# Performance work log

Hardware: AMD Instinct MI355X
Metric: run time of the kernel (lower is better)

The kernel has to match this reference:

```python
import jax, jax.numpy as jnp
import numpy as np

H = 16  # num_heads


def rope_cos_sin(S, d):
    # interleaved RoPE tables: cos = [cos0,cos0,cos1,cos1,...], sin likewise
    pos = jnp.arange(S, dtype=jnp.float32)[:, None]            # [S,1]
    ids = jnp.arange(d // 2, dtype=jnp.float32)
    theta = jnp.power(10000.0, -2.0 * ids / d)                  # [d/2]
    ang = pos * theta                                           # [S,d/2]
    cos = jnp.repeat(jnp.cos(ang), 2, axis=-1)                  # [S,d]
    sin = jnp.repeat(jnp.sin(ang), 2, axis=-1)                  # [S,d]
    return cos, sin


def apply_rope(x, cos, sin):
    # x: [B,H,S,d]; x2 = [-x1, x0, -x3, x2, ...]
    x2 = jnp.stack([-x[..., 1::2], x[..., ::2]], axis=-1).reshape(x.shape)
    return x * cos + x2 * sin


def setup_inputs() -> dict:
    key = jax.random.key(0)
    ks = jax.random.split(key, 9)
    B, S, D = 2, 2048, 1024
    sc = 1.0 / np.sqrt(D)
    return {
        "x": jax.random.normal(ks[0], (B, S, D), dtype=jnp.float32),
        "Wq": jax.random.normal(ks[1], (D, D), dtype=jnp.float32) * sc,
        "bq": jnp.zeros((D,), dtype=jnp.float32),
        "Wk": jax.random.normal(ks[2], (D, D), dtype=jnp.float32) * sc,
        "bk": jnp.zeros((D,), dtype=jnp.float32),
        "Wv": jax.random.normal(ks[3], (D, D), dtype=jnp.float32) * sc,
        "bv": jnp.zeros((D,), dtype=jnp.float32),
        "Wo": jax.random.normal(ks[4], (D, D), dtype=jnp.float32) * sc,
        "bo": jnp.zeros((D,), dtype=jnp.float32),
    }


def reference(x, Wq, bq, Wk, bk, Wv, bv, Wo, bo):
    B, S, D = x.shape
    dk = D // H
    scale = dk ** -0.5  # lsa=False -> fixed scale
    # QKV projections -> [B,H,S,dk]
    q = (x @ Wq + bq).reshape(B, S, H, dk).transpose(0, 2, 1, 3)
    k = (x @ Wk + bk).reshape(B, S, H, dk).transpose(0, 2, 1, 3)
    v = (x @ Wv + bv).reshape(B, S, H, dk).transpose(0, 2, 1, 3)
    cos, sin = rope_cos_sin(S, dk)
    q = apply_rope(q, cos, sin)
    k = apply_rope(k, cos, sin)
    attn_scores = jnp.einsum('bhqd,bhkd->bhqk', q, k) * scale
    attn_weights = jax.nn.softmax(attn_scores, axis=-1)  # dropout p=0
    out = jnp.einsum('bhqk,bhkd->bhqd', attn_weights, v)
    out = out.transpose(0, 2, 1, 3).reshape(B, S, D)
    out = out @ Wo + bo
    return out, attn_weights
```

## Files before the change

### kernel.cpp

```cpp
#include <hip/hip_runtime.h>

typedef __attribute__((ext_vector_type(4))) float f32x4;
typedef __attribute__((ext_vector_type(4))) int   i32x4;
typedef __attribute__((ext_vector_type(8))) short bf16x8;
typedef __attribute__((ext_vector_type(4))) short s16x4;

#define HD 16
#define SQ 2048
#define DM 1024
#define DK 64
#define QSCALE 0.18033688011112042f

__device__ __forceinline__ short f2bf(float f){
  union { float f; unsigned u; } c; c.f = f;
  unsigned r = (c.u + 0x7FFFu + ((c.u >> 16) & 1u)) >> 16;
  return (short)r;
}
__device__ __forceinline__ f32x4 mfma16(bf16x8 a, bf16x8 b, f32x4 c){
  return __builtin_amdgcn_mfma_f32_16x16x32_bf16(a, b, c, 0, 0, 0);
}
__device__ __forceinline__ void gload16(const void* g, void* l){
  __builtin_amdgcn_global_load_lds(
      (const __attribute__((address_space(1))) unsigned*)g,
      (__attribute__((address_space(3))) unsigned*)l, 16, 0, 0);
}


__global__ void k_rope_tab(float2* __restrict__ tab){
  int i = blockIdx.x * 256 + threadIdx.x;
  int s = i >> 5, d2 = i & 31;
  float theta = powf(10000.0f, -(float)d2 / 32.0f);
  float ang = (float)s * theta;
  tab[i] = make_float2(cosf(ang), sinf(ang));
}

__global__ void k_cast(const float* __restrict__ x, short* __restrict__ xb){
  int i = (blockIdx.x * 256 + threadIdx.x) * 4;
  f32x4 v = *(const f32x4*)(x + i);
  s16x4 o;
  o[0] = f2bf(v[0]); o[1] = f2bf(v[1]); o[2] = f2bf(v[2]); o[3] = f2bf(v[3]);
  *(s16x4*)(xb + i) = o;
}

__global__ void k_wt4(const float* __restrict__ W0, const float* __restrict__ W1,
                      const float* __restrict__ W2, const float* __restrict__ W3,
                      short* __restrict__ T0, short* __restrict__ T1,
                      short* __restrict__ T2, short* __restrict__ T3){
  __shared__ float t[32][33];
  const float* W; short* Wt;
  if (blockIdx.z == 0)      { W = W0; Wt = T0; }
  else if (blockIdx.z == 1) { W = W1; Wt = T1; }
  else if (blockIdx.z == 2) { W = W2; Wt = T2; }
  else                      { W = W3; Wt = T3; }
  int kx = blockIdx.x * 32, nx = blockIdx.y * 32;
  int lx = threadIdx.x & 31, ly = threadIdx.x >> 5;
#pragma unroll
  for (int i = 0; i < 32; i += 8)
    t[ly + i][lx] = W[(size_t)(kx + ly + i) * DM + nx + lx];
  __syncthreads();
#pragma unroll
  for (int i = 0; i < 32; i += 8)
    Wt[(size_t)(nx + ly + i) * DM + kx + lx] = f2bf(t[lx][ly + i]);
}

__global__ __launch_bounds__(256) void k_projqkv(const short* __restrict__ A,
    const short* __restrict__ Wqt, const short* __restrict__ Wkt, const short* __restrict__ Wvt,
    const float* __restrict__ bq, const float* __restrict__ bk, const float* __restrict__ bv,
    const float2* __restrict__ rope,
    short* __restrict__ Qo, short* __restrict__ Ko, short* __restrict__ Vo)
{
  __shared__ short As[128 * 64];
  __shared__ short Bs[128 * 64];
  const int mat = blockIdx.y >> 3;
  const int n0 = (blockIdx.y & 7) * 128;
  const short* Bt  = (mat == 0) ? Wqt : (mat == 1) ? Wkt : Wvt;
  const float* bias = (mat == 0) ? bq : (mat == 1) ? bk : bv;
  const int tid = threadIdx.x;
  const int lane = tid & 63, w = tid >> 6;
  const int wr = w >> 1, wc = w & 1;
  const int l15 = lane & 15, l4 = lane >> 4;
  const int m0 = blockIdx.x * 128;
  f32x4 acc[4][4] = {};

  for (int k0 = 0; k0 < DM; k0 += 64) {
#pragma unroll
    for (int i = 0; i < 4; ++i) {
      int c = w * 4 + i;
      int row = c * 8 + (lane >> 3);
      int so = (((lane & 7) * 16) ^ ((row & 7) << 4)) >> 1;
      gload16(A  + (size_t)(m0 + row) * DM + k0 + so, (char*)As + c * 1024);
      gload16(Bt + (size_t)(n0 + row) * DM + k0 + so, (char*)Bs + c * 1024);
    }
    __syncthreads();
#pragma unroll
    for (int kk = 0; kk < 64; kk += 32) {
      bf16x8 af[4], bfr[4];
#pragma unroll
      for (int mi = 0; mi < 4; ++mi) {
        int r = wr * 64 + mi * 16 + l15;
        af[mi] = *(const bf16x8*)((char*)As + ((r * 128 + kk * 2 + l4 * 16) ^ ((r & 7) << 4)));
      }
#pragma unroll
      for (int ni = 0; ni < 4; ++ni) {
        int r = wc * 64 + ni * 16 + l15;
        bfr[ni] = *(const bf16x8*)((char*)Bs + ((r * 128 + kk * 2 + l4 * 16) ^ ((r & 7) << 4)));
      }
#pragma unroll
      for (int mi = 0; mi < 4; ++mi)
#pragma unroll
        for (int ni = 0; ni < 4; ++ni)
          acc[mi][ni] = mfma16(af[mi], bfr[ni], acc[mi][ni]);
    }
    __syncthreads();
  }

#pragma unroll
  for (int mi = 0; mi < 4; ++mi) {
#pragma unroll
    for (int ni = 0; ni < 4; ++ni) {
      int n = n0 + wc * 64 + ni * 16 + l15;
      float bv2 = bias[n];
      if (mat == 2) {
        s16x4 pk;
        int mb = m0 + wr * 64 + mi * 16 + l4 * 4;
#pragma unroll
        for (int r2 = 0; r2 < 4; ++r2) pk[r2] = f2bf(acc[mi][ni][r2] + bv2);
        int b = mb >> 11, s = mb & 2047, h = n >> 6, d = n & 63;
        *(s16x4*)(Vo + ((size_t)((b * HD + h) * DK + d)) * SQ + s) = pk;
      } else {
        short* outp = (mat == 0) ? Qo : Ko;
        float sc = (mat == 0) ? QSCALE : 1.0f;
#pragma unroll
        for (int r2 = 0; r2 < 4; ++r2) {
          int m = m0 + wr * 64 + mi * 16 + l4 * 4 + r2;
          float v = acc[mi][ni][r2] + bv2;
          float pr = __shfl_xor(v, 1);
          int s = m & 2047, d = n & 63;
          float2 cs = rope[(s << 5) + (d >> 1)];
          v = (d & 1) ? (v * cs.x + pr * cs.y) : (v * cs.x - pr * cs.y);
          v *= sc;
          int b = m >> 11, h = n >> 6;
          outp[((size_t)((b * HD + h) * SQ + s)) * DK + d] = f2bf(v);
        }
      }
    }
  }
}

__global__ __launch_bounds__(256) void k_projO(const short* __restrict__ A, const short* __restrict__ Bt,
                                               const float* __restrict__ bias, float* __restrict__ out)
{
  __shared__ short As[64 * 64];
  __shared__ short Bs[128 * 64];
  const int tid = threadIdx.x;
  const int lane = tid & 63, w = tid >> 6;
  const int wr = w >> 1, wc = w & 1;
  const int l15 = lane & 15, l4 = lane >> 4;
  const int m0 = blockIdx.x * 64, n0 = blockIdx.y * 128;
  f32x4 acc[2][4] = {};

  for (int k0 = 0; k0 < DM; k0 += 64) {
#pragma unroll
    for (int i = 0; i < 2; ++i) {
      int c = w * 2 + i;
      int row = c * 8 + (lane >> 3);
      int so = (((lane & 7) * 16) ^ ((row & 7) << 4)) >> 1;
      gload16(A + (size_t)(m0 + row) * DM + k0 + so, (char*)As + c * 1024);
    }
#pragma unroll
    for (int i = 0; i < 4; ++i) {
      int c = w * 4 + i;
      int row = c * 8 + (lane >> 3);
      int so = (((lane & 7) * 16) ^ ((row & 7) << 4)) >> 1;
      gload16(Bt + (size_t)(n0 + row) * DM + k0 + so, (char*)Bs + c * 1024);
    }
    __syncthreads();
#pragma unroll
    for (int kk = 0; kk < 64; kk += 32) {
      bf16x8 af[2], bfr[4];
#pragma unroll
      for (int mi = 0; mi < 2; ++mi) {
        int r = wr * 32 + mi * 16 + l15;
        af[mi] = *(const bf16x8*)((char*)As + ((r * 128 + kk * 2 + l4 * 16) ^ ((r & 7) << 4)));
      }
#pragma unroll
      for (int ni = 0; ni < 4; ++ni) {
        int r = wc * 64 + ni * 16 + l15;
        bfr[ni] = *(const bf16x8*)((char*)Bs + ((r * 128 + kk * 2 + l4 * 16) ^ ((r & 7) << 4)));
      }
#pragma unroll
      for (int mi = 0; mi < 2; ++mi)
#pragma unroll
        for (int ni = 0; ni < 4; ++ni)
          acc[mi][ni] = mfma16(af[mi], bfr[ni], acc[mi][ni]);
    }
    __syncthreads();
  }

#pragma unroll
  for (int mi = 0; mi < 2; ++mi)
#pragma unroll
    for (int ni = 0; ni < 4; ++ni) {
      int n = n0 + wc * 64 + ni * 16 + l15;
      float bv2 = bias[n];
#pragma unroll
      for (int r2 = 0; r2 < 4; ++r2) {
        int m = m0 + wr * 32 + mi * 16 + l4 * 4 + r2;
        out[(size_t)m * DM + n] = acc[mi][ni][r2] + bv2;
      }
    }
}

__global__ __launch_bounds__(256) void k_attn2(const short* __restrict__ Q, const short* __restrict__ K,
    const short* __restrict__ Vt, float* __restrict__ attn_out, short* __restrict__ ctx)
{
  __shared__ short Qs[128 * 64];
  __shared__ short Ks[128 * 64];
  __shared__ short Vs[64 * 128];
  __shared__ short Ps[128 * 128];
  const int bh = blockIdx.y, qt = blockIdx.x;
  const int tid = threadIdx.x, lane = tid & 63, w = tid >> 6;
  const int l15 = lane & 15, l4 = lane >> 4;
  const short* Qg = Q + (size_t)(bh * SQ + qt * 128) * DK;
  const short* Kg = K + (size_t)bh * SQ * DK;
  const short* Vg = Vt + (size_t)bh * DK * SQ;

#pragma unroll
  for (int i = 0; i < 4; ++i) {
    int c = w * 4 + i;
    int row = c * 8 + (lane >> 3);
    int so = (((lane & 7) * 16) ^ ((row & 7) << 4)) >> 1;
    gload16(Qg + row * 64 + so, (char*)Qs + c * 1024);
  }

  float rs[2][4] = {};
  for (int kt = 0; kt < 16; ++kt) {
#pragma unroll
    for (int i = 0; i < 4; ++i) {
      int c = w * 4 + i;
      int row = c * 8 + (lane >> 3);
      int so = (((lane & 7) * 16) ^ ((row & 7) << 4)) >> 1;
      gload16(Kg + (size_t)(kt * 128 + row) * 64 + so, (char*)Ks + c * 1024);
    }
    __syncthreads();
    f32x4 p[2][8] = {};
#pragma unroll
    for (int kk = 0; kk < 64; kk += 32) {
      bf16x8 aq[2];
#pragma unroll
      for (int mi = 0; mi < 2; ++mi) {
        int r = w * 32 + mi * 16 + l15;
        aq[mi] = *(const bf16x8*)((char*)Qs + ((r * 128 + kk * 2 + l4 * 16) ^ ((r & 7) << 4)));
      }
#pragma unroll
      for (int ni = 0; ni < 8; ++ni) {
        int r = ni * 16 + l15;
        bf16x8 bk = *(const bf16x8*)((char*)Ks + ((r * 128 + kk * 2 + l4 * 16) ^ ((r & 7) << 4)));
        p[0][ni] = mfma16(aq[0], bk, p[0][ni]);
        p[1][ni] = mfma16(aq[1], bk, p[1][ni]);
      }
    }
#pragma unroll
    for (int mi = 0; mi < 2; ++mi)
#pragma unroll
      for (int ni = 0; ni < 8; ++ni)
#pragma unroll
        for (int r2 = 0; r2 < 4; ++r2)
          rs[mi][r2] += exp2f(p[mi][ni][r2]);
    __syncthreads();
  }
  float rinv_r[2][4];
#pragma unroll
  for (int mi = 0; mi < 2; ++mi)
#pragma unroll
    for (int r2 = 0; r2 < 4; ++r2) {
      float v = rs[mi][r2];
      v += __shfl_xor(v, 1); v += __shfl_xor(v, 2);
      v += __shfl_xor(v, 4); v += __shfl_xor(v, 8);
      rinv_r[mi][r2] = 1.0f / v;
    }

  f32x4 c[2][4] = {};
  float* attn_base = attn_out + ((size_t)(bh * SQ + qt * 128)) * SQ;

  for (int kt = 0; kt < 16; ++kt) {
#pragma unroll
    for (int i = 0; i < 4; ++i) {
      int c2 = w * 4 + i;
      int row = c2 * 8 + (lane >> 3);
      int so = (((lane & 7) * 16) ^ ((row & 7) << 4)) >> 1;
      gload16(Kg + (size_t)(kt * 128 + row) * 64 + so, (char*)Ks + c2 * 1024);
    }
#pragma unroll
    for (int i = 0; i < 4; ++i) {
      int c2 = w * 4 + i;
      int row = c2 * 4 + (lane >> 4);
      int so = (((lane & 15) * 16) ^ ((row & 15) << 4)) >> 1;
      gload16(Vg + (size_t)row * SQ + kt * 128 + so, (char*)Vs + c2 * 1024);
    }
    __syncthreads();
    f32x4 p[2][8] = {};
#pragma unroll
    for (int kk = 0; kk < 64; kk += 32) {
      bf16x8 aq[2];
#pragma unroll
      for (int mi = 0; mi < 2; ++mi) {
        int r = w * 32 + mi * 16 + l15;
        aq[mi] = *(const bf16x8*)((char*)Qs + ((r * 128 + kk * 2 + l4 * 16) ^ ((r & 7) << 4)));
      }
#pragma unroll
      for (int ni = 0; ni < 8; ++ni) {
        int r = ni * 16 + l15;
        bf16x8 bk = *(const bf16x8*)((char*)Ks + ((r * 128 + kk * 2 + l4 * 16) ^ ((r & 7) << 4)));
        p[0][ni] = mfma16(aq[0], bk, p[0][ni]);
        p[1][ni] = mfma16(aq[1], bk, p[1][ni]);
      }
    }
#pragma unroll
    for (int mi = 0; mi < 2; ++mi)
#pragma unroll
      for (int ni = 0; ni < 8; ++ni)
#pragma unroll
        for (int r2 = 0; r2 < 4; ++r2) {
          int row = w * 32 + mi * 16 + l4 * 4 + r2;
          int col = ni * 16 + l15;
          float wgt = exp2f(p[mi][ni][r2]) * rinv_r[mi][r2];
          attn_base[(size_t)row * SQ + kt * 128 + col] = wgt;
          *(short*)((char*)Ps + ((row * 256 + col * 2) ^ ((row & 15) << 4))) = f2bf(wgt);
        }
#pragma unroll
    for (int kk = 0; kk < 128; kk += 32) {
      bf16x8 ap[2];
#pragma unroll
      for (int mi = 0; mi < 2; ++mi) {
        int r = w * 32 + mi * 16 + l15;
        ap[mi] = *(const bf16x8*)((char*)Ps + ((r * 256 + kk * 2 + l4 * 16) ^ ((r & 15) << 4)));
      }
#pragma unroll
      for (int ni = 0; ni < 4; ++ni) {
        int r = ni * 16 + l15;
        bf16x8 bv = *(const bf16x8*)((char*)Vs + ((r * 256 + kk * 2 + l4 * 16) ^ ((r & 15) << 4)));
        c[0][ni] = mfma16(ap[0], bv, c[0][ni]);
        c[1][ni] = mfma16(ap[1], bv, c[1][ni]);
      }
    }
    __syncthreads();
  }
  int b = bh >> 4, h = bh & 15;
#pragma unroll
  for (int mi = 0; mi < 2; ++mi)
#pragma unroll
    for (int ni = 0; ni < 4; ++ni)
#pragma unroll
      for (int r2 = 0; r2 < 4; ++r2) {
        int s = qt * 128 + w * 32 + mi * 16 + l4 * 4 + r2;
        int d = ni * 16 + l15;
        ctx[((size_t)(b * SQ + s)) * DM + h * DK + d] = f2bf(c[mi][ni][r2]);
      }
}

extern "C" void kernel_launch(void* const* d_in, const int* in_sizes, int n_in,
                              void* d_out, int out_size, void* d_ws, size_t ws_size,
                              hipStream_t stream)
{
  const float* x  = (const float*)d_in[0];
  const float* Wq = (const float*)d_in[1];
  const float* bq = (const float*)d_in[2];
  const float* Wk = (const float*)d_in[3];
  const float* bk = (const float*)d_in[4];
  const float* Wv = (const float*)d_in[5];
  const float* bv = (const float*)d_in[6];
  const float* Wo = (const float*)d_in[7];
  const float* bo = (const float*)d_in[8];

  char* p = (char*)d_ws;
  float2* rope = (float2*)p;  p += (size_t)SQ * 32 * sizeof(float2);
  short* xb  = (short*)p;     p += (size_t)4096 * DM * 2;
  short* Wqt = (short*)p;     p += (size_t)DM * DM * 2;
  short* Wkt = (short*)p;     p += (size_t)DM * DM * 2;
  short* Wvt = (short*)p;     p += (size_t)DM * DM * 2;
  short* Wot = (short*)p;     p += (size_t)DM * DM * 2;
  short* Qr  = (short*)p;     p += (size_t)2 * HD * SQ * DK * 2;
  short* Kr  = (short*)p;     p += (size_t)2 * HD * SQ * DK * 2;
  short* Vtr = (short*)p;     p += (size_t)2 * HD * SQ * DK * 2;
  short* ctx = (short*)p;     p += (size_t)4096 * DM * 2;

  k_rope_tab<<<SQ * 32 / 256, 256, 0, stream>>>(rope);
  k_cast<<<4096 * DM / 1024, 256, 0, stream>>>(x, xb);
  k_wt4<<<dim3(32, 32, 4), 256, 0, stream>>>(Wq, Wk, Wv, Wo, Wqt, Wkt, Wvt, Wot);
  k_projqkv<<<dim3(32, 24), 256, 0, stream>>>(xb, Wqt, Wkt, Wvt, bq, bk, bv, rope, Qr, Kr, Vtr);
  float* attn = (float*)d_out + (size_t)2 * SQ * DM;
  k_attn2<<<dim3(16, 32), 256, 0, stream>>>(Qr, Kr, Vtr, attn, ctx);
  k_projO<<<dim3(64, 8), 256, 0, stream>>>(ctx, Wot, bo, (float*)d_out);
}
```

Before: 326.2 us.

## Drop LDS staging in attention, load Q/K/V directly and vectorize weight stores

Q fragments are loaded once into registers, and K and V tiles are read straight from global memory instead of being staged in shared memory. This removes the block-wide barriers; the probability tile in shared memory is now only touched by the wave that owns its rows. The MFMA operand order is swapped (K as A, Q as B) so each lane holds four consecutive key columns of one query row. That allows 16-byte stores of the float attention weights and packed 8-byte bf16 writes into shared memory, replacing scalar stores. Row sums now reduce across lane groups with two shuffles instead of four. The cost is that each wave reads K and V from global itself rather than sharing one copy per block, which depends on cache hits.

```diff
diff --git a/kernel.cpp b/kernel.cpp
--- a/kernel.cpp
+++ b/kernel.cpp
@@ -214,9 +214,6 @@
 __global__ __launch_bounds__(256) void k_attn2(const short* __restrict__ Q, const short* __restrict__ K,
     const short* __restrict__ Vt, float* __restrict__ attn_out, short* __restrict__ ctx)
 {
-  __shared__ short Qs[128 * 64];
-  __shared__ short Ks[128 * 64];
-  __shared__ short Vs[64 * 128];
   __shared__ short Ps[128 * 128];
   const int bh = blockIdx.y, qt = blockIdx.x;
   const int tid = threadIdx.x, lane = tid & 63, w = tid >> 6;
@@ -225,109 +222,70 @@
   const short* Kg = K + (size_t)bh * SQ * DK;
   const short* Vg = Vt + (size_t)bh * DK * SQ;
 
-#pragma unroll
-  for (int i = 0; i < 4; ++i) {
-    int c = w * 4 + i;
-    int row = c * 8 + (lane >> 3);
-    int so = (((lane & 7) * 16) ^ ((row & 7) << 4)) >> 1;
-    gload16(Qg + row * 64 + so, (char*)Qs + c * 1024);
-  }
-
-  float rs[2][4] = {};
+  bf16x8 q_b[2][2];
+#pragma unroll
+  for (int mi = 0; mi < 2; ++mi)
+#pragma unroll
+    for (int kx = 0; kx < 2; ++kx)
+      q_b[mi][kx] = *(const bf16x8*)(Qg + (w * 32 + mi * 16 + l15) * 64 + kx * 32 + l4 * 8);
+
+  float rs[2] = {0.0f, 0.0f};
   for (int kt = 0; kt < 16; ++kt) {
-#pragma unroll
-    for (int i = 0; i < 4; ++i) {
-      int c = w * 4 + i;
-      int row = c * 8 + (lane >> 3);
-      int so = (((lane & 7) * 16) ^ ((row & 7) << 4)) >> 1;
-      gload16(Kg + (size_t)(kt * 128 + row) * 64 + so, (char*)Ks + c * 1024);
-    }
-    __syncthreads();
-    f32x4 p[2][8] = {};
-#pragma unroll
-    for (int kk = 0; kk < 64; kk += 32) {
-      bf16x8 aq[2];
-#pragma unroll
-      for (int mi = 0; mi < 2; ++mi) {
-        int r = w * 32 + mi * 16 + l15;
-        aq[mi] = *(const bf16x8*)((char*)Qs + ((r * 128 + kk * 2 + l4 * 16) ^ ((r & 7) << 4)));
-      }
-#pragma unroll
-      for (int ni = 0; ni < 8; ++ni) {
-        int r = ni * 16 + l15;
-        bf16x8 bk = *(const bf16x8*)((char*)Ks + ((r * 128 + kk * 2 + l4 * 16) ^ ((r & 7) << 4)));
-        p[0][ni] = mfma16(aq[0], bk, p[0][ni]);
-        p[1][ni] = mfma16(aq[1], bk, p[1][ni]);
-      }
-    }
-#pragma unroll
-    for (int mi = 0; mi < 2; ++mi)
-#pragma unroll
-      for (int ni = 0; ni < 8; ++ni)
-#pragma unroll
-        for (int r2 = 0; r2 < 4; ++r2)
-          rs[mi][r2] += exp2f(p[mi][ni][r2]);
-    __syncthreads();
-  }
-  float rinv_r[2][4];
-#pragma unroll
-  for (int mi = 0; mi < 2; ++mi)
-#pragma unroll
-    for (int r2 = 0; r2 < 4; ++r2) {
-      float v = rs[mi][r2];
-      v += __shfl_xor(v, 1); v += __shfl_xor(v, 2);
-      v += __shfl_xor(v, 4); v += __shfl_xor(v, 8);
-      rinv_r[mi][r2] = 1.0f / v;
-    }
+    const short* Kt = Kg + (size_t)kt * 128 * DK;
+#pragma unroll
+    for (int ni = 0; ni < 8; ++ni) {
+      f32x4 p0 = {}, p1 = {};
+#pragma unroll
+      for (int kx = 0; kx < 2; ++kx) {
+        bf16x8 ka = *(const bf16x8*)(Kt + (ni * 16 + l15) * 64 + kx * 32 + l4 * 8);
+        p0 = mfma16(ka, q_b[0][kx], p0);
+        p1 = mfma16(ka, q_b[1][kx], p1);
+      }
+#pragma unroll
+      for (int r2 = 0; r2 < 4; ++r2) {
+        rs[0] += exp2f(p0[r2]);
+        rs[1] += exp2f(p1[r2]);
+      }
+    }
+  }
+  float rinv[2];
+#pragma unroll
+  for (int mi = 0; mi < 2; ++mi) {
+    float v = rs[mi];
+    v += __shfl_xor(v, 16);
+    v += __shfl_xor(v, 32);
+    rinv[mi] = 1.0f / v;
+  }
 
   f32x4 c[2][4] = {};
   float* attn_base = attn_out + ((size_t)(bh * SQ + qt * 128)) * SQ;
 
   for (int kt = 0; kt < 16; ++kt) {
-#pragma unroll
-    for (int i = 0; i < 4; ++i) {
-      int c2 = w * 4 + i;
-      int row = c2 * 8 + (lane >> 3);
-      int so = (((lane & 7) * 16) ^ ((row & 7) << 4)) >> 1;
-      gload16(Kg + (size_t)(kt * 128 + row) * 64 + so, (char*)Ks + c2 * 1024);
-    }
-#pragma unroll
-    for (int i = 0; i < 4; ++i) {
-      int c2 = w * 4 + i;
-      int row = c2 * 4 + (lane >> 4);
-      int so = (((lane & 15) * 16) ^ ((row & 15) << 4)) >> 1;
-      gload16(Vg + (size_t)row * SQ + kt * 128 + so, (char*)Vs + c2 * 1024);
-    }
-    __syncthreads();
-    f32x4 p[2][8] = {};
-#pragma unroll
-    for (int kk = 0; kk < 64; kk += 32) {
-      bf16x8 aq[2];
+    const short* Kt = Kg + (size_t)kt * 128 * DK;
+#pragma unroll
+    for (int ni = 0; ni < 8; ++ni) {
+      f32x4 p0 = {}, p1 = {};
+#pragma unroll
+      for (int kx = 0; kx < 2; ++kx) {
+        bf16x8 ka = *(const bf16x8*)(Kt + (ni * 16 + l15) * 64 + kx * 32 + l4 * 8);
+        p0 = mfma16(ka, q_b[0][kx], p0);
+        p1 = mfma16(ka, q_b[1][kx], p1);
+      }
 #pragma unroll
       for (int mi = 0; mi < 2; ++mi) {
-        int r = w * 32 + mi * 16 + l15;
-        aq[mi] = *(const bf16x8*)((char*)Qs + ((r * 128 + kk * 2 + l4 * 16) ^ ((r & 7) << 4)));
-      }
-#pragma unroll
-      for (int ni = 0; ni < 8; ++ni) {
-        int r = ni * 16 + l15;
-        bf16x8 bk = *(const bf16x8*)((char*)Ks + ((r * 128 + kk * 2 + l4 * 16) ^ ((r & 7) << 4)));
-        p[0][ni] = mfma16(aq[0], bk, p[0][ni]);
-        p[1][ni] = mfma16(aq[1], bk, p[1][ni]);
-      }
-    }
-#pragma unroll
-    for (int mi = 0; mi < 2; ++mi)
-#pragma unroll
-      for (int ni = 0; ni < 8; ++ni)
+        f32x4 pp = mi ? p1 : p0;
+        int q = w * 32 + mi * 16 + l15;
+        f32x4 wv;
+        s16x4 pk;
 #pragma unroll
         for (int r2 = 0; r2 < 4; ++r2) {
-          int row = w * 32 + mi * 16 + l4 * 4 + r2;
-          int col = ni * 16 + l15;
-          float wgt = exp2f(p[mi][ni][r2]) * rinv_r[mi][r2];
-          attn_base[(size_t)row * SQ + kt * 128 + col] = wgt;
-          *(short*)((char*)Ps + ((row * 256 + col * 2) ^ ((row & 15) << 4))) = f2bf(wgt);
+          wv[r2] = exp2f(pp[r2]) * rinv[mi];
+          pk[r2] = f2bf(wv[r2]);
         }
+        *(f32x4*)(attn_base + (size_t)q * SQ + kt * 128 + ni * 16 + l4 * 4) = wv;
+        *(s16x4*)((char*)Ps + ((q * 256 + ni * 32 + l4 * 8) ^ ((q & 15) << 4))) = pk;
+      }
+    }
 #pragma unroll
     for (int kk = 0; kk < 128; kk += 32) {
       bf16x8 ap[2];
@@ -337,25 +295,23 @@
         ap[mi] = *(const bf16x8*)((char*)Ps + ((r * 256 + kk * 2 + l4 * 16) ^ ((r & 15) << 4)));
       }
 #pragma unroll
-      for (int ni = 0; ni < 4; ++ni) {
-        int r = ni * 16 + l15;
-        bf16x8 bv = *(const bf16x8*)((char*)Vs + ((r * 256 + kk * 2 + l4 * 16) ^ ((r & 15) << 4)));
-        c[0][ni] = mfma16(ap[0], bv, c[0][ni]);
-        c[1][ni] = mfma16(ap[1], bv, c[1][ni]);
-      }
-    }
-    __syncthreads();
+      for (int nd = 0; nd < 4; ++nd) {
+        bf16x8 bv = *(const bf16x8*)(Vg + (size_t)(nd * 16 + l15) * SQ + kt * 128 + kk + l4 * 8);
+        c[0][nd] = mfma16(ap[0], bv, c[0][nd]);
+        c[1][nd] = mfma16(ap[1], bv, c[1][nd]);
+      }
+    }
   }
   int b = bh >> 4, h = bh & 15;
 #pragma unroll
   for (int mi = 0; mi < 2; ++mi)
 #pragma unroll
-    for (int ni = 0; ni < 4; ++ni)
+    for (int nd = 0; nd < 4; ++nd)
 #pragma unroll
       for (int r2 = 0; r2 < 4; ++r2) {
         int s = qt * 128 + w * 32 + mi * 16 + l4 * 4 + r2;
-        int d = ni * 16 + l15;
-        ctx[((size_t)(b * SQ + s)) * DM + h * DK + d] = f2bf(c[mi][ni][r2]);
+        int d = nd * 16 + l15;
+        ctx[((size_t)(b * SQ + s)) * DM + h * DK + d] = f2bf(c[mi][nd][r2]);
       }
 }
 
```

Measured after the change: 501.3 us. +53.7%, slower.
